# Performance work log

Hardware: AMD Instinct MI355X
Metric: run time of the kernel (lower is better)

Reference implementation:

```python
import jax, jax.numpy as jnp
import numpy as np

N_USERS = 100000
N_ITEMS = 50000
N_NODES = N_USERS + N_ITEMS
D = 64
N_LAYERS = 3
POP_BINS = 10
NNZ = 2000000
BATCH = 256
BIAS_SCALE = 1.0


def setup_inputs() -> dict:
    key = jax.random.key(0)
    ks = jax.random.split(key, 16)
    std = 0.01
    inp = {
        "user_emb": jax.random.normal(ks[0], (N_USERS, D), jnp.float32) * std,
        "item_emb": jax.random.normal(ks[1], (N_ITEMS, D), jnp.float32) * std,
        "user_bias": jnp.zeros((N_USERS, 1), jnp.float32),
        "item_bias": jnp.zeros((N_ITEMS, 1), jnp.float32),
        "pop_emb": jax.random.normal(ks[2], (POP_BINS, D), jnp.float32) * std,
        "uW1": jax.random.normal(ks[3], (D, D), jnp.float32) / np.sqrt(D),
        "ub1": jnp.zeros((D,), jnp.float32),
        "uW2": jax.random.normal(ks[4], (D, D), jnp.float32) / np.sqrt(D),
        "ub2": jnp.zeros((D,), jnp.float32),
        "iW1": jax.random.normal(ks[5], (D, D), jnp.float32) / np.sqrt(D),
        "ib1": jnp.zeros((D,), jnp.float32),
        "iW2": jax.random.normal(ks[6], (D, D), jnp.float32) / np.sqrt(D),
        "ib2": jnp.zeros((D,), jnp.float32),
        "gW1": jax.random.normal(ks[7], (2 * D, D), jnp.float32) / np.sqrt(2 * D),
        "gb1": jnp.zeros((D,), jnp.float32),
        "gW2": jax.random.normal(ks[8], (D, 1), jnp.float32) / np.sqrt(D),
        "gb2": jnp.zeros((1,), jnp.float32),
        "adj_vals": jax.random.uniform(ks[9], (NNZ,), jnp.float32),
        "adj_rows": jax.random.randint(ks[10], (NNZ,), 0, N_NODES, jnp.int32),
        "adj_cols": jax.random.randint(ks[11], (NNZ,), 0, N_NODES, jnp.int32),
        "item_pop_bins": jax.random.randint(ks[12], (N_ITEMS,), 0, POP_BINS, jnp.int32),
        "users": jax.random.randint(ks[13], (BATCH,), 0, N_USERS, jnp.int32),
    }
    return inp


def _spmm(vals, rows, cols, E):
    # sparse (N x N) @ E  via gather + segment-sum
    msgs = vals[:, None] * E[cols]          # [nnz, d]
    return jax.ops.segment_sum(msgs, rows, num_segments=N_NODES)


def _mlp2(x, W1, b1, W2, b2):
    return jax.nn.relu(x @ W1 + b1) @ W2 + b2


def reference(user_emb, item_emb, user_bias, item_bias, pop_emb,
              uW1, ub1, uW2, ub2, iW1, ib1, iW2, ib2,
              gW1, gb1, gW2, gb2,
              adj_vals, adj_rows, adj_cols, item_pop_bins, users):
    # ---- computer(): LightGCN propagation with uniform layer weights ----
    emb = jnp.concatenate([user_emb, item_emb], axis=0)   # [N, d]
    w = 1.0 / (N_LAYERS + 1)
    out = emb * w
    cur = emb
    for _ in range(N_LAYERS):
        cur = _spmm(adj_vals, adj_rows, adj_cols, cur)
        out = out + cur * w
    all_users, all_items = out[:N_USERS], out[N_USERS:]

    # ---- popularity-gated item fusion ----
    p_vec = pop_emb[item_pop_bins]                         # [n_items, d]
    gate_in = jnp.concatenate([all_items, p_vec], axis=-1)
    z = jax.nn.sigmoid(_mlp2(gate_in, gW1, gb1, gW2, gb2)) # [n_items, 1]
    items_fused = (1.0 - z) * all_items + z * p_vec

    # ---- two-tower scoring over all items ----
    U = _mlp2(all_users[users], uW1, ub1, uW2, ub2)        # [B, d]
    I = _mlp2(items_fused, iW1, ib1, iW2, ib2)             # [n_items, d]
    scores = U @ I.T                                        # [B, n_items]
    scores = scores + user_bias[users] * BIAS_SCALE + (item_bias.T) * BIAS_SCALE
    return scores
```

## Files before the change

### kernel.cpp

```cpp
#include <hip/hip_runtime.h>
#include <hip/hip_fp16.h>

#define N_USERS 100000
#define N_ITEMS 50000
#define N_NODES 150000
#define D 64
#define NNZ 2000000
#define BATCH 256
#define POP_BINS 10

#define BSH 9
#define NB2 293
#define CAP 8192
#define P1_EPB 4096
#define P1_BLOCKS 489

#define ST_P 130

__global__ __launch_bounds__(256) void k_bcount(const int* __restrict__ rows,
                                                int* __restrict__ bcnt) {
  __shared__ int c[NB2];
  int t = threadIdx.x;
  for (int i = t; i < NB2; i += 256) c[i] = 0;
  __syncthreads();
  int base = blockIdx.x * P1_EPB;
  for (int i = 0; i < 16; i++) {
    int e = base + i * 256 + t;
    if (e < NNZ) atomicAdd(&c[rows[e] >> BSH], 1);
  }
  __syncthreads();
  for (int i = t; i < NB2; i += 256)
    if (c[i]) atomicAdd(&bcnt[i], c[i]);
}

__global__ __launch_bounds__(512) void k_bscan(int* __restrict__ bcnt) {
  __shared__ int s[512];
  int t = threadIdx.x;
  int v = (t < NB2) ? bcnt[t] : 0;
  s[t] = v;
  __syncthreads();
  for (int o = 1; o < 512; o <<= 1) {
    int x = (t >= o) ? s[t - o] : 0;
    __syncthreads();
    s[t] += x;
    __syncthreads();
  }
  if (t < NB2) bcnt[t] = s[t] - v;
}

__global__ __launch_bounds__(256) void k_p1(const int* __restrict__ rows,
                                            const int* __restrict__ cols,
                                            const float* __restrict__ vals,
                                            int* __restrict__ bcur,
                                            uint2* __restrict__ gstage) {
  __shared__ int cnt[NB2];
  __shared__ int gbase[NB2];
  int t = threadIdx.x;
  for (int i = t; i < NB2; i += 256) cnt[i] = 0;
  __syncthreads();
  int base = blockIdx.x * P1_EPB;
  for (int i = 0; i < 16; i++) {
    int e = base + i * 256 + t;
    if (e < NNZ) atomicAdd(&cnt[rows[e] >> BSH], 1);
  }
  __syncthreads();
  for (int i = t; i < NB2; i += 256) {
    int c = cnt[i];
    gbase[i] = c ? atomicAdd(&bcur[i], c) : 0;
    cnt[i] = 0;
  }
  __syncthreads();
  for (int i = 0; i < 16; i++) {
    int e = base + i * 256 + t;
    if (e < NNZ) {
      int r = rows[e];
      int b = r >> BSH;
      int rank = atomicAdd(&cnt[b], 1);
      unsigned key = ((unsigned)(r & 511) << 18) | (unsigned)cols[e];
      gstage[gbase[b] + rank] = make_uint2(key, __float_as_uint(vals[e]));
    }
  }
}

__global__ __launch_bounds__(256) void k_p2(const int* __restrict__ bcur,
                                            const uint2* __restrict__ gstage,
                                            uint2* __restrict__ epack,
                                            int* __restrict__ rowptr) {
  __shared__ int cnt[512];
  __shared__ int off[512];
  __shared__ int s[256];
  __shared__ uint2 buf[CAP];
  int b = blockIdx.x, t = threadIdx.x;
  int base = (b == 0) ? 0 : bcur[b - 1];
  int end = bcur[b];
  int n = end - base;
  cnt[t] = 0;
  cnt[t + 256] = 0;
  __syncthreads();
  for (int j = t; j < n; j += 256)
    atomicAdd(&cnt[gstage[base + j].x >> 18], 1);
  __syncthreads();
  int c0 = cnt[2 * t], c1 = cnt[2 * t + 1];
  s[t] = c0 + c1;
  __syncthreads();
  for (int o = 1; o < 256; o <<= 1) {
    int x = (t >= o) ? s[t - o] : 0;
    __syncthreads();
    s[t] += x;
    __syncthreads();
  }
  int ex = t ? s[t - 1] : 0;
  off[2 * t] = ex;
  off[2 * t + 1] = ex + c0;
  int gr = (b << BSH) + 2 * t;
  if (gr < N_NODES) rowptr[gr] = base + ex;
  if (gr + 1 < N_NODES) rowptr[gr + 1] = base + ex + c0;
  if (b == NB2 - 1 && t == 0) rowptr[N_NODES] = NNZ;
  __syncthreads();
  for (int j = t; j < n; j += 256) {
    uint2 ed = gstage[base + j];
    int lr = ed.x >> 18;
    int pos = atomicAdd(&off[lr], 1);
    buf[pos] = make_uint2(ed.x & 0x3FFFFu, ed.y);
  }
  __syncthreads();
  for (int j = t; j < n; j += 256) epack[base + j] = buf[j];
}

__global__ __launch_bounds__(256) void k_flags(const int* __restrict__ users,
                                               int* __restrict__ uflag,
                                               int* __restrict__ ulist,
                                               int* __restrict__ ucnt) {
  int u = users[threadIdx.x];
  if (atomicExch(&uflag[u], 1) == 0) {
    int p = atomicAdd(ucnt, 1);
    ulist[p] = u;
  }
}

__global__ __launch_bounds__(256) void k_cvt(const float* __restrict__ ue,
                                             const float* __restrict__ ie,
                                             __half* __restrict__ Eh) {
  int t = blockIdx.x * 256 + threadIdx.x;
  if (t >= 2400000) return;
  size_t fo = (size_t)t * 4;
  const float* src = (fo < (size_t)N_USERS * 64) ? ue + fo
                                                 : ie + (fo - (size_t)N_USERS * 64);
  float4 v = *(const float4*)src;
  __half2* dst = (__half2*)(Eh + fo);
  dst[0] = __floats2half2_rn(v.x, v.y);
  dst[1] = __floats2half2_rn(v.z, v.w);
}

#define SPMM_QW_BODY(TBL)                                                     \
  float a0 = 0.f, a1 = 0.f, a2 = 0.f, a3 = 0.f;                               \
  int j = beg;                                                                \
  for (; j + 7 < end; j += 8) {                                               \
    uint2 ea = epack[j + q];                                                  \
    uint2 eb = epack[j + 4 + q];                                              \
    uint2 ra = *(const uint2*)(TBL + (size_t)ea.x * 64 + 4 * p);              \
    uint2 rb = *(const uint2*)(TBL + (size_t)eb.x * 64 + 4 * p);              \
    float va = __uint_as_float(ea.y), vb = __uint_as_float(eb.y);             \
    float2 la = __half22float2(*(const __half2*)&ra.x);                       \
    float2 ha = __half22float2(*(const __half2*)&ra.y);                       \
    float2 lb = __half22float2(*(const __half2*)&rb.x);                       \
    float2 hb = __half22float2(*(const __half2*)&rb.y);                       \
    a0 += va * la.x; a1 += va * la.y; a2 += va * ha.x; a3 += va * ha.y;       \
    a0 += vb * lb.x; a1 += vb * lb.y; a2 += vb * hb.x; a3 += vb * hb.y;       \
  }                                                                           \
  for (; j < end; j += 4) {                                                   \
    int jj = j + q;                                                           \
    int jc = (jj < end) ? jj : end - 1;                                       \
    uint2 e = epack[jc];                                                      \
    float v = (jj < end) ? __uint_as_float(e.y) : 0.f;                        \
    uint2 r = *(const uint2*)(TBL + (size_t)e.x * 64 + 4 * p);                \
    float2 l = __half22float2(*(const __half2*)&r.x);                         \
    float2 h2 = __half22float2(*(const __half2*)&r.y);                        \
    a0 += v * l.x; a1 += v * l.y; a2 += v * h2.x; a3 += v * h2.y;             \
  }                                                                           \
  a0 += __shfl_xor(a0, 16, 64); a0 += __shfl_xor(a0, 32, 64);                 \
  a1 += __shfl_xor(a1, 16, 64); a1 += __shfl_xor(a1, 32, 64);                 \
  a2 += __shfl_xor(a2, 16, 64); a2 += __shfl_xor(a2, 32, 64);                 \
  a3 += __shfl_xor(a3, 16, 64); a3 += __shfl_xor(a3, 32, 64);

__global__ __launch_bounds__(256) void k_spmm1(const int* __restrict__ rowptr,
                                               const uint2* __restrict__ epack,
                                               const float* __restrict__ ue,
                                               const float* __restrict__ ie,
                                               const __half* __restrict__ Eh0,
                                               const int* __restrict__ uflag,
                                               __half* __restrict__ EoutH,
                                               float* __restrict__ Oacc) {
  int wave = blockIdx.x * 4 + (threadIdx.x >> 6);
  int row = __builtin_amdgcn_readfirstlane(wave);
  if (row >= N_NODES) return;
  int lane = threadIdx.x & 63;
  int p = lane & 15, q = lane >> 4;
  int beg = rowptr[row];
  int end = rowptr[row + 1];
  SPMM_QW_BODY(Eh0)
  if (q == 0) {
    __half2* eo = (__half2*)(EoutH + (size_t)row * 64 + 4 * p);
    eo[0] = __floats2half2_rn(a0, a1);
    eo[1] = __floats2half2_rn(a2, a3);
    bool need = (row >= N_USERS) || (uflag[row] != 0);
    if (need) {
      const float* srow = (row < N_USERS) ? ue + (size_t)row * 64
                                          : ie + (size_t)(row - N_USERS) * 64;
      float4 sv = *(const float4*)(srow + 4 * p);
      *(float4*)(Oacc + (size_t)row * 64 + 4 * p) =
          make_float4(0.25f * (sv.x + a0), 0.25f * (sv.y + a1),
                      0.25f * (sv.z + a2), 0.25f * (sv.w + a3));
    }
  }
}

__global__ __launch_bounds__(256) void k_spmm2h(const int* __restrict__ rowptr,
                                                const uint2* __restrict__ epack,
                                                const __half* __restrict__ Ein,
                                                const int* __restrict__ uflag,
                                                __half* __restrict__ EoutH,
                                                float* __restrict__ Oacc) {
  int wave = blockIdx.x * 4 + (threadIdx.x >> 6);
  int row = __builtin_amdgcn_readfirstlane(wave);
  if (row >= N_NODES) return;
  int lane = threadIdx.x & 63;
  int p = lane & 15, q = lane >> 4;
  int beg = rowptr[row];
  int end = rowptr[row + 1];
  SPMM_QW_BODY(Ein)
  if (q == 0) {
    __half2* eo = (__half2*)(EoutH + (size_t)row * 64 + 4 * p);
    eo[0] = __floats2half2_rn(a0, a1);
    eo[1] = __floats2half2_rn(a2, a3);
    if (row >= N_USERS || uflag[row] != 0) {
      float4* op = (float4*)(Oacc + (size_t)row * 64 + 4 * p);
      float4 cur = *op;
      *op = make_float4(cur.x + 0.25f * a0, cur.y + 0.25f * a1,
                        cur.z + 0.25f * a2, cur.w + 0.25f * a3);
    }
  }
}

__global__ __launch_bounds__(256) void k_spmm3h(const int* __restrict__ rowptr,
                                                const uint2* __restrict__ epack,
                                                const __half* __restrict__ Ein,
                                                const int* __restrict__ ulist,
                                                const int* __restrict__ ucnt,
                                                float* __restrict__ Oacc) {
  int w = blockIdx.x * 4 + (threadIdx.x >> 6);
  int row;
  if (w < N_ITEMS) {
    row = N_USERS + w;
  } else {
    int k = w - N_ITEMS;
    if (k >= ucnt[0]) return;
    row = ulist[k];
  }
  row = __builtin_amdgcn_readfirstlane(row);
  int lane = threadIdx.x & 63;
  int p = lane & 15, q = lane >> 4;
  int beg = rowptr[row];
  int end = rowptr[row + 1];
  SPMM_QW_BODY(Ein)
  if (q == 0) {
    float4* op = (float4*)(Oacc + (size_t)row * 64 + 4 * p);
    float4 cur = *op;
    *op = make_float4(cur.x + 0.25f * a0, cur.y + 0.25f * a1,
                      cur.z + 0.25f * a2, cur.w + 0.25f * a3);
  }
}

__global__ __launch_bounds__(256) void k_wt(const float* __restrict__ uW1,
                                            float* __restrict__ WT) {
  int t = blockIdx.x * 256 + threadIdx.x;
  if (t < 4096) {
    int o = t >> 6, k = t & 63;
    WT[t] = uW1[k * 64 + o];
  }
}

__global__ __launch_bounds__(256) void k_pw(const float* __restrict__ pop,
                                            const float* __restrict__ gW1,
                                            const float* __restrict__ iW1,
                                            float* __restrict__ hp,
                                            float* __restrict__ pp1) {
  for (int idx = threadIdx.x; idx < 2 * POP_BINS * 64; idx += 256) {
    int q = idx;
    bool second = q >= POP_BINS * 64;
    if (second) q -= POP_BINS * 64;
    int b = q >> 6, o = q & 63;
    float s = 0.f;
    if (!second) {
      for (int k = 0; k < 64; k++) s += pop[b * 64 + k] * gW1[(64 + k) * 64 + o];
      hp[q] = s;
    } else {
      for (int k = 0; k < 64; k++) s += pop[b * 64 + k] * iW1[k * 64 + o];
      pp1[q] = s;
    }
  }
}

__global__ __launch_bounds__(64) void k_user(const float* __restrict__ Oacc,
                                             const int* __restrict__ users,
                                             const float* __restrict__ ubias,
                                             const float* __restrict__ uW1T,
                                             const float* __restrict__ ub1,
                                             const float* __restrict__ uW2,
                                             const float* __restrict__ ub2,
                                             float* __restrict__ Ut) {
  int b = blockIdx.x * 64 + threadIdx.x;
  int u = users[b];
  float x[64];
  const float4* xr = (const float4*)(Oacc + (size_t)u * 64);
#pragma unroll
  for (int q = 0; q < 16; q++) {
    float4 t4 = xr[q];
    x[4 * q] = t4.x; x[4 * q + 1] = t4.y; x[4 * q + 2] = t4.z; x[4 * q + 3] = t4.w;
  }
  float acc[64];
#pragma unroll
  for (int o2 = 0; o2 < 64; o2++) acc[o2] = ub2[o2];
#pragma unroll 1
  for (int o = 0; o < 64; o++) {
    const float* w = uW1T + o * 64;
    float a0 = ub1[o], a1 = 0.f, a2 = 0.f, a3 = 0.f;
#pragma unroll
    for (int k = 0; k < 64; k += 4) {
      a0 += x[k] * w[k]; a1 += x[k + 1] * w[k + 1];
      a2 += x[k + 2] * w[k + 2]; a3 += x[k + 3] * w[k + 3];
    }
    float hv = a0 + a1 + a2 + a3;
    hv = hv > 0.f ? hv : 0.f;
    const float* w2 = uW2 + o * 64;
#pragma unroll
    for (int o2 = 0; o2 < 64; o2++) acc[o2] += hv * w2[o2];
  }
#pragma unroll
  for (int o2 = 0; o2 < 64; o2++) Ut[o2 * 256 + b] = acc[o2];
  Ut[64 * 256 + b] = ubias[u];
}

__global__ __launch_bounds__(256) void k_gemm1z(const float* __restrict__ Oacc,
                                                const float* __restrict__ gW1,
                                                const float* __restrict__ iW1,
                                                const int* __restrict__ bins,
                                                const float* __restrict__ hp,
                                                const float* __restrict__ pp1,
                                                const float* __restrict__ gb1,
                                                const float* __restrict__ gW2,
                                                const float* __restrict__ gb2,
                                                const float* __restrict__ ib1,
                                                float* __restrict__ H1) {
  __shared__ float Is[64 * ST_P];
  __shared__ float Bs[64 * 128];
  __shared__ float zp[128][9];
  __shared__ float zs[128];
  int tid = threadIdx.x;
  int i0 = blockIdx.x * 128;
  {
    int c4 = tid & 15, r0 = tid >> 4;
#pragma unroll
    for (int s = 0; s < 8; s++) {
      int r = r0 + s * 16;
      int it = i0 + r;
      float4 v = make_float4(0.f, 0.f, 0.f, 0.f);
      if (it < N_ITEMS) v = *(const float4*)(Oacc + (size_t)(N_USERS + it) * 64 + c4 * 4);
      Is[(c4 * 4 + 0) * ST_P + r] = v.x;
      Is[(c4 * 4 + 1) * ST_P + r] = v.y;
      Is[(c4 * 4 + 2) * ST_P + r] = v.z;
      Is[(c4 * 4 + 3) * ST_P + r] = v.w;
    }
  }
  for (int idx = tid; idx < 64 * 128; idx += 256) {
    int k = idx >> 7, o = idx & 127;
    Bs[idx] = (o < 64) ? gW1[k * 64 + o] : iW1[k * 64 + (o - 64)];
  }
  __syncthreads();
  int tx = tid & 15, ty = tid >> 4;
  float acc[8][8];
#pragma unroll
  for (int a = 0; a < 8; a++)
#pragma unroll
    for (int b = 0; b < 8; b++) acc[a][b] = 0.f;
  const float* ip = Is + tx * 8;
  const float* wp = Bs + ty * 8;
#pragma unroll 2
  for (int k = 0; k < 64; k++) {
    float4 iv0 = *(const float4*)(ip + k * ST_P);
    float4 iv1 = *(const float4*)(ip + k * ST_P + 4);
    float4 wv0 = *(const float4*)(wp + k * 128);
    float4 wv1 = *(const float4*)(wp + k * 128 + 4);
    float iv[8] = {iv0.x, iv0.y, iv0.z, iv0.w, iv1.x, iv1.y, iv1.z, iv1.w};
    float wv[8] = {wv0.x, wv0.y, wv0.z, wv0.w, wv1.x, wv1.y, wv1.z, wv1.w};
#pragma unroll
    for (int a = 0; a < 8; a++)
#pragma unroll
      for (int b = 0; b < 8; b++) acc[a][b] += iv[a] * wv[b];
  }
  int ibase = i0 + tx * 8;
  if (ty < 8) {
    int o0 = ty * 8;
#pragma unroll
    for (int a = 0; a < 8; a++) {
      int it = ibase + a;
      float p = 0.f;
      if (it < N_ITEMS) {
        int bin = bins[it];
        const float* hpr = hp + bin * 64 + o0;
#pragma unroll
        for (int b = 0; b < 8; b++) {
          float g = acc[a][b] + hpr[b] + gb1[o0 + b];
          g = g > 0.f ? g : 0.f;
          p += g * gW2[o0 + b];
        }
      }
      zp[tx * 8 + a][ty] = p;
    }
  }
  __syncthreads();
  if (tid < 128) {
    float s = gb2[0];
#pragma unroll
    for (int k = 0; k < 8; k++) s += zp[tid][k];
    zs[tid] = 1.f / (1.f + expf(-s));
  }
  __syncthreads();
  if (ty >= 8) {
    int o0 = (ty - 8) * 8;
#pragma unroll
    for (int a = 0; a < 8; a++) {
      int it = ibase + a;
      if (it < N_ITEMS) {
        float z = zs[tx * 8 + a];
        int bin = bins[it];
        const float* ppr = pp1 + bin * 64 + o0;
        float h[8];
#pragma unroll
        for (int b = 0; b < 8; b++) {
          float v = (1.f - z) * acc[a][b] + z * ppr[b] + ib1[o0 + b];
          h[b] = v > 0.f ? v : 0.f;
        }
        *(float4*)(H1 + (size_t)it * 64 + o0) = make_float4(h[0], h[1], h[2], h[3]);
        *(float4*)(H1 + (size_t)it * 64 + o0 + 4) = make_float4(h[4], h[5], h[6], h[7]);
      }
    }
  }
}

__global__ __launch_bounds__(256) void k_gemm2(const float* __restrict__ H1,
                                               const float* __restrict__ iW2,
                                               const float* __restrict__ ib2,
                                               float* __restrict__ I) {
  __shared__ float Is[64 * ST_P];
  __shared__ float Bs[64 * 64];
  int tid = threadIdx.x;
  int i0 = blockIdx.x * 128;
  {
    int c4 = tid & 15, r0 = tid >> 4;
#pragma unroll
    for (int s = 0; s < 8; s++) {
      int r = r0 + s * 16;
      int it = i0 + r;
      float4 v = make_float4(0.f, 0.f, 0.f, 0.f);
      if (it < N_ITEMS) v = *(const float4*)(H1 + (size_t)it * 64 + c4 * 4);
      Is[(c4 * 4 + 0) * ST_P + r] = v.x;
      Is[(c4 * 4 + 1) * ST_P + r] = v.y;
      Is[(c4 * 4 + 2) * ST_P + r] = v.z;
      Is[(c4 * 4 + 3) * ST_P + r] = v.w;
    }
  }
  for (int idx = tid; idx < 64 * 64; idx += 256) Bs[idx] = iW2[idx];
  __syncthreads();
  int tx = tid & 15, ty = tid >> 4;
  float acc[8][4];
#pragma unroll
  for (int a = 0; a < 8; a++)
#pragma unroll
    for (int b = 0; b < 4; b++) acc[a][b] = 0.f;
  const float* ip = Is + tx * 8;
  const float* wp = Bs + ty * 4;
#pragma unroll 2
  for (int k = 0; k < 64; k++) {
    float4 iv0 = *(const float4*)(ip + k * ST_P);
    float4 iv1 = *(const float4*)(ip + k * ST_P + 4);
    float4 wv = *(const float4*)(wp + k * 64);
    float iv[8] = {iv0.x, iv0.y, iv0.z, iv0.w, iv1.x, iv1.y, iv1.z, iv1.w};
    float wvv[4] = {wv.x, wv.y, wv.z, wv.w};
#pragma unroll
    for (int a = 0; a < 8; a++)
#pragma unroll
      for (int b = 0; b < 4; b++) acc[a][b] += iv[a] * wvv[b];
  }
  int ibase = i0 + tx * 8;
  int oc = ty * 4;
  float b0 = ib2[oc], b1 = ib2[oc + 1], b2 = ib2[oc + 2], b3 = ib2[oc + 3];
#pragma unroll
  for (int a = 0; a < 8; a++) {
    int it = ibase + a;
    if (it < N_ITEMS) {
      float4 s0 = make_float4(acc[a][0] + b0, acc[a][1] + b1,
                              acc[a][2] + b2, acc[a][3] + b3);
      *(float4*)(I + (size_t)it * 64 + oc) = s0;
    }
  }
}

__global__ __launch_bounds__(256) void k_scores(const float* __restrict__ I,
                                                const float* __restrict__ Ut,
                                                const float* __restrict__ item_bias,
                                                float* __restrict__ out) {
  __shared__ float Is[64 * ST_P];
  __shared__ float Us[64 * 128];
  int tid = threadIdx.x;
  int i0 = blockIdx.x * 128;
  int ubase = blockIdx.y * 128;
  {
    int c4 = tid & 15, r0 = tid >> 4;
#pragma unroll
    for (int s = 0; s < 8; s++) {
      int r = r0 + s * 16;
      int it = i0 + r;
      float4 v = make_float4(0.f, 0.f, 0.f, 0.f);
      if (it < N_ITEMS) v = *(const float4*)(I + (size_t)it * 64 + c4 * 4);
      Is[(c4 * 4 + 0) * ST_P + r] = v.x;
      Is[(c4 * 4 + 1) * ST_P + r] = v.y;
      Is[(c4 * 4 + 2) * ST_P + r] = v.z;
      Is[(c4 * 4 + 3) * ST_P + r] = v.w;
    }
  }
  {
    int u4 = tid & 31, k0 = tid >> 5;
#pragma unroll
    for (int s = 0; s < 8; s++) {
      int k = k0 + s * 8;
      float4 v = *(const float4*)(Ut + k * 256 + ubase + u4 * 4);
      *(float4*)(Us + k * 128 + u4 * 4) = v;
    }
  }
  __syncthreads();
  int tx = tid & 15;
  int ty = tid >> 4;
  float acc[8][8];
#pragma unroll
  for (int a = 0; a < 8; a++)
#pragma unroll
    for (int b = 0; b < 8; b++) acc[a][b] = 0.f;
  const float* ip = Is + tx * 8;
  const float* up = Us + ty * 8;
#pragma unroll 2
  for (int k = 0; k < 64; k++) {
    float4 iv0 = *(const float4*)(ip + k * ST_P);
    float4 iv1 = *(const float4*)(ip + k * ST_P + 4);
    float4 uv0 = *(const float4*)(up + k * 128);
    float4 uv1 = *(const float4*)(up + k * 128 + 4);
    float iv[8] = {iv0.x, iv0.y, iv0.z, iv0.w, iv1.x, iv1.y, iv1.z, iv1.w};
    float uv[8] = {uv0.x, uv0.y, uv0.z, uv0.w, uv1.x, uv1.y, uv1.z, uv1.w};
#pragma unroll
    for (int a = 0; a < 8; a++)
#pragma unroll
      for (int b = 0; b < 8; b++) acc[a][b] += iv[a] * uv[b];
  }
  int ibase = i0 + tx * 8;
  float ib[8];
#pragma unroll
  for (int a = 0; a < 8; a++)
    ib[a] = (ibase + a < N_ITEMS) ? item_bias[ibase + a] : 0.f;
#pragma unroll
  for (int bb = 0; bb < 8; bb++) {
    int bu = ubase + ty * 8 + bb;
    float ubias = Ut[64 * 256 + bu];
    float* orow = out + (size_t)bu * N_ITEMS + ibase;
    if (ibase + 7 < N_ITEMS) {
      float4 s0 = make_float4(acc[0][bb] + ubias + ib[0], acc[1][bb] + ubias + ib[1],
                              acc[2][bb] + ubias + ib[2], acc[3][bb] + ubias + ib[3]);
      float4 s1 = make_float4(acc[4][bb] + ubias + ib[4], acc[5][bb] + ubias + ib[5],
                              acc[6][bb] + ubias + ib[6], acc[7][bb] + ubias + ib[7]);
      *(float4*)orow = s0;
      *(float4*)(orow + 4) = s1;
    } else {
#pragma unroll
      for (int a = 0; a < 8; a++)
        if (ibase + a < N_ITEMS) orow[a] = acc[a][bb] + ubias + ib[a];
    }
  }
}

extern "C" void kernel_launch(void* const* d_in, const int* in_sizes, int n_in,
                              void* d_out, int out_size, void* d_ws, size_t ws_size,
                              hipStream_t stream) {
  const float* user_emb  = (const float*)d_in[0];
  const float* item_emb  = (const float*)d_in[1];
  const float* user_bias = (const float*)d_in[2];
  const float* item_bias = (const float*)d_in[3];
  const float* pop_emb   = (const float*)d_in[4];
  const float* uW1 = (const float*)d_in[5];
  const float* ub1 = (const float*)d_in[6];
  const float* uW2 = (const float*)d_in[7];
  const float* ub2 = (const float*)d_in[8];
  const float* iW1 = (const float*)d_in[9];
  const float* ib1 = (const float*)d_in[10];
  const float* iW2 = (const float*)d_in[11];
  const float* ib2 = (const float*)d_in[12];
  const float* gW1 = (const float*)d_in[13];
  const float* gb1 = (const float*)d_in[14];
  const float* gW2 = (const float*)d_in[15];
  const float* gb2 = (const float*)d_in[16];
  const float* adj_vals = (const float*)d_in[17];
  const int* adj_rows = (const int*)d_in[18];
  const int* adj_cols = (const int*)d_in[19];
  const int* bins  = (const int*)d_in[20];
  const int* users = (const int*)d_in[21];
  float* out = (float*)d_out;

  float* ws = (float*)d_ws;
  float* Oacc = ws;
  float* bufA = ws + 9600000;
  float* bufB = ws + 19200000;
  uint2* epack = (uint2*)(ws + 28800000);
  int* rowptr = (int*)(ws + 32800000);
  int* uflag  = (int*)(ws + 32960000);
  int* ucnt   = (int*)(ws + 33060000);
  int* ulist  = (int*)(ws + 33061000);
  float* Ut   = ws + 33130000;
  float* WT   = ws + 33150000;
  float* hp   = ws + 33160000;
  float* pp1  = ws + 33161000;
  int* bcur   = (int*)(ws + 33170000);
  uint2* gstage = (uint2*)bufB;
  __half* Eh0 = (__half*)bufA;
  __half* E1h = (__half*)(bufA + 4800000);
  __half* E2h = (__half*)bufB;
  float* H1 = bufA + 6400000;
  float* I  = bufB;
  const float* uW1T = WT;

  hipMemsetAsync(bcur, 0, NB2 * sizeof(int), stream);
  hipMemsetAsync(uflag, 0, 100001 * sizeof(int), stream);
  k_cvt<<<9375, 256, 0, stream>>>(user_emb, item_emb, Eh0);
  k_bcount<<<P1_BLOCKS, 256, 0, stream>>>(adj_rows, bcur);
  k_bscan<<<1, 512, 0, stream>>>(bcur);
  k_p1<<<P1_BLOCKS, 256, 0, stream>>>(adj_rows, adj_cols, adj_vals, bcur, gstage);
  k_p2<<<NB2, 256, 0, stream>>>(bcur, gstage, epack, rowptr);
  k_flags<<<1, 256, 0, stream>>>(users, uflag, ulist, ucnt);

  k_spmm1<<<37500, 256, 0, stream>>>(rowptr, epack, user_emb, item_emb, Eh0, uflag, E1h, Oacc);
  k_spmm2h<<<37500, 256, 0, stream>>>(rowptr, epack, E1h, uflag, E2h, Oacc);
  k_spmm3h<<<12564, 256, 0, stream>>>(rowptr, epack, E2h, ulist, ucnt, Oacc);

  k_wt<<<16, 256, 0, stream>>>(uW1, WT);
  k_pw<<<1, 256, 0, stream>>>(pop_emb, gW1, iW1, hp, pp1);
  k_user<<<4, 64, 0, stream>>>(Oacc, users, user_bias, uW1T, ub1, uW2, ub2, Ut);
  k_gemm1z<<<391, 256, 0, stream>>>(Oacc, gW1, iW1, bins, hp, pp1, gb1, gW2, gb2, ib1, H1);
  k_gemm2<<<391, 256, 0, stream>>>(H1, iW2, ib2, I);
  k_scores<<<dim3(391, 2), 256, 0, stream>>>(I, Ut, item_bias, out);
}
```

Before: 554.7 us.

## Drop bucket count pass, prefetch SpMM edges deeply, bitmask flags, wave-parallel user MLP

```diff
diff --git a/kernel.cpp b/kernel.cpp
--- a/kernel.cpp
+++ b/kernel.cpp
@@ -16,37 +16,7 @@
 #define P1_BLOCKS 489
 
 #define ST_P 130
-
-__global__ __launch_bounds__(256) void k_bcount(const int* __restrict__ rows,
-                                                int* __restrict__ bcnt) {
-  __shared__ int c[NB2];
-  int t = threadIdx.x;
-  for (int i = t; i < NB2; i += 256) c[i] = 0;
-  __syncthreads();
-  int base = blockIdx.x * P1_EPB;
-  for (int i = 0; i < 16; i++) {
-    int e = base + i * 256 + t;
-    if (e < NNZ) atomicAdd(&c[rows[e] >> BSH], 1);
-  }
-  __syncthreads();
-  for (int i = t; i < NB2; i += 256)
-    if (c[i]) atomicAdd(&bcnt[i], c[i]);
-}
-
-__global__ __launch_bounds__(512) void k_bscan(int* __restrict__ bcnt) {
-  __shared__ int s[512];
-  int t = threadIdx.x;
-  int v = (t < NB2) ? bcnt[t] : 0;
-  s[t] = v;
-  __syncthreads();
-  for (int o = 1; o < 512; o <<= 1) {
-    int x = (t >= o) ? s[t - o] : 0;
-    __syncthreads();
-    s[t] += x;
-    __syncthreads();
-  }
-  if (t < NB2) bcnt[t] = s[t] - v;
-}
+#define MAXC 7
 
 __global__ __launch_bounds__(256) void k_p1(const int* __restrict__ rows,
                                             const int* __restrict__ cols,
@@ -77,7 +47,8 @@
       int b = r >> BSH;
       int rank = atomicAdd(&cnt[b], 1);
       unsigned key = ((unsigned)(r & 511) << 18) | (unsigned)cols[e];
-      gstage[gbase[b] + rank] = make_uint2(key, __float_as_uint(vals[e]));
+      gstage[(size_t)b * CAP + gbase[b] + rank] =
+          make_uint2(key, __float_as_uint(vals[e]));
     }
   }
 }
@@ -85,20 +56,23 @@
 __global__ __launch_bounds__(256) void k_p2(const int* __restrict__ bcur,
                                             const uint2* __restrict__ gstage,
                                             uint2* __restrict__ epack,
-                                            int* __restrict__ rowptr) {
+                                            int* __restrict__ rowbeg,
+                                            int* __restrict__ rowend,
+                                            int* __restrict__ gcursor) {
   __shared__ int cnt[512];
   __shared__ int off[512];
   __shared__ int s[256];
+  __shared__ int gbs;
   __shared__ uint2 buf[CAP];
   int b = blockIdx.x, t = threadIdx.x;
-  int base = (b == 0) ? 0 : bcur[b - 1];
-  int end = bcur[b];
-  int n = end - base;
+  int n = bcur[b];
+  const uint2* gs = gstage + (size_t)b * CAP;
+  if (t == 0) gbs = atomicAdd(gcursor, n);
   cnt[t] = 0;
   cnt[t + 256] = 0;
   __syncthreads();
   for (int j = t; j < n; j += 256)
-    atomicAdd(&cnt[gstage[base + j].x >> 18], 1);
+    atomicAdd(&cnt[gs[j].x >> 18], 1);
   __syncthreads();
   int c0 = cnt[2 * t], c1 = cnt[2 * t + 1];
   s[t] = c0 + c1;
@@ -112,13 +86,13 @@
   int ex = t ? s[t - 1] : 0;
   off[2 * t] = ex;
   off[2 * t + 1] = ex + c0;
+  int base = gbs;
   int gr = (b << BSH) + 2 * t;
-  if (gr < N_NODES) rowptr[gr] = base + ex;
-  if (gr + 1 < N_NODES) rowptr[gr + 1] = base + ex + c0;
-  if (b == NB2 - 1 && t == 0) rowptr[N_NODES] = NNZ;
+  if (gr < N_NODES) { rowbeg[gr] = base + ex; rowend[gr] = base + ex + c0; }
+  if (gr + 1 < N_NODES) { rowbeg[gr + 1] = base + ex + c0; rowend[gr + 1] = base + ex + c0 + c1; }
   __syncthreads();
   for (int j = t; j < n; j += 256) {
-    uint2 ed = gstage[base + j];
+    uint2 ed = gs[j];
     int lr = ed.x >> 18;
     int pos = atomicAdd(&off[lr], 1);
     buf[pos] = make_uint2(ed.x & 0x3FFFFu, ed.y);
@@ -132,7 +106,8 @@
                                                int* __restrict__ ulist,
                                                int* __restrict__ ucnt) {
   int u = users[threadIdx.x];
-  if (atomicExch(&uflag[u], 1) == 0) {
+  int old = atomicOr(&uflag[u >> 5], 1 << (u & 31));
+  if (!((old >> (u & 31)) & 1)) {
     int p = atomicAdd(ucnt, 1);
     ulist[p] = u;
   }
@@ -152,38 +127,55 @@
   dst[1] = __floats2half2_rn(v.z, v.w);
 }
 
-#define SPMM_QW_BODY(TBL)                                                     \
+#define SPMM_DEEP(TBL)                                                        \
+  int n = end - beg;                                                          \
+  int nc = (n + 3) >> 2;                                                      \
+  if (nc > MAXC) nc = MAXC;                                                   \
+  uint2 ed[MAXC];                                                             \
+  _Pragma("unroll")                                                           \
+  for (int c = 0; c < MAXC; c++) {                                            \
+    if (c < nc) {                                                             \
+      int jj = beg + 4 * c + q;                                               \
+      int jc = jj < end ? jj : end - 1;                                       \
+      ed[c] = epack[jc];                                                      \
+    }                                                                         \
+  }                                                                           \
+  uint2 rg[MAXC]; float rv[MAXC];                                             \
+  _Pragma("unroll")                                                           \
+  for (int c = 0; c < MAXC; c++) {                                            \
+    if (c < nc) {                                                             \
+      int jj = beg + 4 * c + q;                                               \
+      rv[c] = (jj < end) ? __uint_as_float(ed[c].y) : 0.f;                    \
+      rg[c] = *(const uint2*)(TBL + (size_t)ed[c].x * 64 + 4 * p);            \
+    }                                                                         \
+  }                                                                           \
   float a0 = 0.f, a1 = 0.f, a2 = 0.f, a3 = 0.f;                               \
-  int j = beg;                                                                \
-  for (; j + 7 < end; j += 8) {                                               \
-    uint2 ea = epack[j + q];                                                  \
-    uint2 eb = epack[j + 4 + q];                                              \
-    uint2 ra = *(const uint2*)(TBL + (size_t)ea.x * 64 + 4 * p);              \
-    uint2 rb = *(const uint2*)(TBL + (size_t)eb.x * 64 + 4 * p);              \
-    float va = __uint_as_float(ea.y), vb = __uint_as_float(eb.y);             \
-    float2 la = __half22float2(*(const __half2*)&ra.x);                       \
-    float2 ha = __half22float2(*(const __half2*)&ra.y);                       \
-    float2 lb = __half22float2(*(const __half2*)&rb.x);                       \
-    float2 hb = __half22float2(*(const __half2*)&rb.y);                       \
-    a0 += va * la.x; a1 += va * la.y; a2 += va * ha.x; a3 += va * ha.y;       \
-    a0 += vb * lb.x; a1 += vb * lb.y; a2 += vb * hb.x; a3 += vb * hb.y;       \
+  _Pragma("unroll")                                                           \
+  for (int c = 0; c < MAXC; c++) {                                            \
+    if (c < nc) {                                                             \
+      float2 lo = __half22float2(*(const __half2*)&rg[c].x);                  \
+      float2 hi = __half22float2(*(const __half2*)&rg[c].y);                  \
+      a0 += rv[c] * lo.x; a1 += rv[c] * lo.y;                                 \
+      a2 += rv[c] * hi.x; a3 += rv[c] * hi.y;                                 \
+    }                                                                         \
   }                                                                           \
-  for (; j < end; j += 4) {                                                   \
+  for (int j = beg + 4 * MAXC; j < end; j += 4) {   \
     int jj = j + q;                                                           \
-    int jc = (jj < end) ? jj : end - 1;                                       \
+    int jc = jj < end ? jj : end - 1;                                         \
     uint2 e = epack[jc];                                                      \
     float v = (jj < end) ? __uint_as_float(e.y) : 0.f;                        \
     uint2 r = *(const uint2*)(TBL + (size_t)e.x * 64 + 4 * p);                \
-    float2 l = __half22float2(*(const __half2*)&r.x);                         \
-    float2 h2 = __half22float2(*(const __half2*)&r.y);                        \
-    a0 += v * l.x; a1 += v * l.y; a2 += v * h2.x; a3 += v * h2.y;             \
+    float2 lo = __half22float2(*(const __half2*)&r.x);                        \
+    float2 hi = __half22float2(*(const __half2*)&r.y);                        \
+    a0 += v * lo.x; a1 += v * lo.y; a2 += v * hi.x; a3 += v * hi.y;           \
   }                                                                           \
   a0 += __shfl_xor(a0, 16, 64); a0 += __shfl_xor(a0, 32, 64);                 \
   a1 += __shfl_xor(a1, 16, 64); a1 += __shfl_xor(a1, 32, 64);                 \
   a2 += __shfl_xor(a2, 16, 64); a2 += __shfl_xor(a2, 32, 64);                 \
   a3 += __shfl_xor(a3, 16, 64); a3 += __shfl_xor(a3, 32, 64);
 
-__global__ __launch_bounds__(256) void k_spmm1(const int* __restrict__ rowptr,
+__global__ __launch_bounds__(256) void k_spmm1(const int* __restrict__ rowbeg,
+                                               const int* __restrict__ rowend,
                                                const uint2* __restrict__ epack,
                                                const float* __restrict__ ue,
                                                const float* __restrict__ ie,
@@ -196,14 +188,14 @@
   if (row >= N_NODES) return;
   int lane = threadIdx.x & 63;
   int p = lane & 15, q = lane >> 4;
-  int beg = rowptr[row];
-  int end = rowptr[row + 1];
-  SPMM_QW_BODY(Eh0)
+  int beg = rowbeg[row];
+  int end = rowend[row];
+  SPMM_DEEP(Eh0)
   if (q == 0) {
     __half2* eo = (__half2*)(EoutH + (size_t)row * 64 + 4 * p);
     eo[0] = __floats2half2_rn(a0, a1);
     eo[1] = __floats2half2_rn(a2, a3);
-    bool need = (row >= N_USERS) || (uflag[row] != 0);
+    bool need = (row >= N_USERS) || (((uflag[row >> 5] >> (row & 31)) & 1) != 0);
     if (need) {
       const float* srow = (row < N_USERS) ? ue + (size_t)row * 64
                                           : ie + (size_t)(row - N_USERS) * 64;
@@ -215,7 +207,8 @@
   }
 }
 
-__global__ __launch_bounds__(256) void k_spmm2h(const int* __restrict__ rowptr,
+__global__ __launch_bounds__(256) void k_spmm2h(const int* __restrict__ rowbeg,
+                                                const int* __restrict__ rowend,
                                                 const uint2* __restrict__ epack,
                                                 const __half* __restrict__ Ein,
                                                 const int* __restrict__ uflag,
@@ -226,14 +219,14 @@
   if (row >= N_NODES) return;
   int lane = threadIdx.x & 63;
   int p = lane & 15, q = lane >> 4;
-  int beg = rowptr[row];
-  int end = rowptr[row + 1];
-  SPMM_QW_BODY(Ein)
+  int beg = rowbeg[row];
+  int end = rowend[row];
+  SPMM_DEEP(Ein)
   if (q == 0) {
     __half2* eo = (__half2*)(EoutH + (size_t)row * 64 + 4 * p);
     eo[0] = __floats2half2_rn(a0, a1);
     eo[1] = __floats2half2_rn(a2, a3);
-    if (row >= N_USERS || uflag[row] != 0) {
+    if (row >= N_USERS || (((uflag[row >> 5] >> (row & 31)) & 1) != 0)) {
       float4* op = (float4*)(Oacc + (size_t)row * 64 + 4 * p);
       float4 cur = *op;
       *op = make_float4(cur.x + 0.25f * a0, cur.y + 0.25f * a1,
@@ -242,7 +235,8 @@
   }
 }
 
-__global__ __launch_bounds__(256) void k_spmm3h(const int* __restrict__ rowptr,
+__global__ __launch_bounds__(256) void k_spmm3h(const int* __restrict__ rowbeg,
+                                                const int* __restrict__ rowend,
                                                 const uint2* __restrict__ epack,
                                                 const __half* __restrict__ Ein,
                                                 const int* __restrict__ ulist,
@@ -260,23 +254,14 @@
   row = __builtin_amdgcn_readfirstlane(row);
   int lane = threadIdx.x & 63;
   int p = lane & 15, q = lane >> 4;
-  int beg = rowptr[row];
-  int end = rowptr[row + 1];
-  SPMM_QW_BODY(Ein)
+  int beg = rowbeg[row];
+  int end = rowend[row];
+  SPMM_DEEP(Ein)
   if (q == 0) {
     float4* op = (float4*)(Oacc + (size_t)row * 64 + 4 * p);
     float4 cur = *op;
     *op = make_float4(cur.x + 0.25f * a0, cur.y + 0.25f * a1,
                       cur.z + 0.25f * a2, cur.w + 0.25f * a3);
-  }
-}
-
-__global__ __launch_bounds__(256) void k_wt(const float* __restrict__ uW1,
-                                            float* __restrict__ WT) {
-  int t = blockIdx.x * 256 + threadIdx.x;
-  if (t < 4096) {
-    int o = t >> 6, k = t & 63;
-    WT[t] = uW1[k * 64 + o];
   }
 }
 
@@ -301,44 +286,29 @@
   }
 }
 
-__global__ __launch_bounds__(64) void k_user(const float* __restrict__ Oacc,
-                                             const int* __restrict__ users,
-                                             const float* __restrict__ ubias,
-                                             const float* __restrict__ uW1T,
-                                             const float* __restrict__ ub1,
-                                             const float* __restrict__ uW2,
-                                             const float* __restrict__ ub2,
-                                             float* __restrict__ Ut) {
-  int b = blockIdx.x * 64 + threadIdx.x;
-  int u = users[b];
-  float x[64];
-  const float4* xr = (const float4*)(Oacc + (size_t)u * 64);
-#pragma unroll
-  for (int q = 0; q < 16; q++) {
-    float4 t4 = xr[q];
-    x[4 * q] = t4.x; x[4 * q + 1] = t4.y; x[4 * q + 2] = t4.z; x[4 * q + 3] = t4.w;
-  }
-  float acc[64];
-#pragma unroll
-  for (int o2 = 0; o2 < 64; o2++) acc[o2] = ub2[o2];
-#pragma unroll 1
-  for (int o = 0; o < 64; o++) {
-    const float* w = uW1T + o * 64;
-    float a0 = ub1[o], a1 = 0.f, a2 = 0.f, a3 = 0.f;
-#pragma unroll
-    for (int k = 0; k < 64; k += 4) {
-      a0 += x[k] * w[k]; a1 += x[k + 1] * w[k + 1];
-      a2 += x[k + 2] * w[k + 2]; a3 += x[k + 3] * w[k + 3];
-    }
-    float hv = a0 + a1 + a2 + a3;
-    hv = hv > 0.f ? hv : 0.f;
-    const float* w2 = uW2 + o * 64;
-#pragma unroll
-    for (int o2 = 0; o2 < 64; o2++) acc[o2] += hv * w2[o2];
-  }
-#pragma unroll
-  for (int o2 = 0; o2 < 64; o2++) Ut[o2 * 256 + b] = acc[o2];
-  Ut[64 * 256 + b] = ubias[u];
+__global__ __launch_bounds__(256) void k_user(const float* __restrict__ Oacc,
+                                              const int* __restrict__ users,
+                                              const float* __restrict__ ubias,
+                                              const float* __restrict__ uW1,
+                                              const float* __restrict__ ub1,
+                                              const float* __restrict__ uW2,
+                                              const float* __restrict__ ub2,
+                                              float* __restrict__ Ut) {
+  int ub = blockIdx.x * 4 + (threadIdx.x >> 6);
+  int lane = threadIdx.x & 63;
+  int u = users[ub];
+  float x = Oacc[(size_t)u * 64 + lane];
+  float h = ub1[lane];
+#pragma unroll
+  for (int k = 0; k < 64; k++)
+    h = fmaf(__shfl(x, k, 64), uW1[k * 64 + lane], h);
+  h = h > 0.f ? h : 0.f;
+  float o = ub2[lane];
+#pragma unroll
+  for (int k = 0; k < 64; k++)
+    o = fmaf(__shfl(h, k, 64), uW2[k * 64 + lane], o);
+  Ut[lane * 256 + ub] = o;
+  if (lane == 0) Ut[64 * 256 + ub] = ubias[u];
 }
 
 __global__ __launch_bounds__(256) void k_gemm1z(const float* __restrict__ Oacc,
@@ -618,39 +588,36 @@
   float* bufA = ws + 9600000;
   float* bufB = ws + 19200000;
   uint2* epack = (uint2*)(ws + 28800000);
-  int* rowptr = (int*)(ws + 32800000);
-  int* uflag  = (int*)(ws + 32960000);
-  int* ucnt   = (int*)(ws + 33060000);
-  int* ulist  = (int*)(ws + 33061000);
-  float* Ut   = ws + 33130000;
-  float* WT   = ws + 33150000;
-  float* hp   = ws + 33160000;
-  float* pp1  = ws + 33161000;
-  int* bcur   = (int*)(ws + 33170000);
+  int* rowbeg = (int*)(ws + 32800000);
+  int* rowend = (int*)(ws + 32950000);
+  int* uflag  = (int*)(ws + 33100000);
+  int* ucnt   = (int*)(ws + 33103125);
+  int* ulist  = (int*)(ws + 33103130);
+  float* Ut   = ws + 33104000;
+  float* hp   = ws + 33121000;
+  float* pp1  = ws + 33122000;
+  int* bcur   = (int*)(ws + 33123000);
+  int* gcursor = (int*)(ws + 33123293);
   uint2* gstage = (uint2*)bufB;
   __half* Eh0 = (__half*)bufA;
   __half* E1h = (__half*)(bufA + 4800000);
   __half* E2h = (__half*)bufB;
   float* H1 = bufA + 6400000;
   float* I  = bufB;
-  const float* uW1T = WT;
-
-  hipMemsetAsync(bcur, 0, NB2 * sizeof(int), stream);
-  hipMemsetAsync(uflag, 0, 100001 * sizeof(int), stream);
+
+  hipMemsetAsync(bcur, 0, 294 * sizeof(int), stream);
+  hipMemsetAsync(uflag, 0, 3126 * sizeof(int), stream);
   k_cvt<<<9375, 256, 0, stream>>>(user_emb, item_emb, Eh0);
-  k_bcount<<<P1_BLOCKS, 256, 0, stream>>>(adj_rows, bcur);
-  k_bscan<<<1, 512, 0, stream>>>(bcur);
   k_p1<<<P1_BLOCKS, 256, 0, stream>>>(adj_rows, adj_cols, adj_vals, bcur, gstage);
-  k_p2<<<NB2, 256, 0, stream>>>(bcur, gstage, epack, rowptr);
+  k_p2<<<NB2, 256, 0, stream>>>(bcur, gstage, epack, rowbeg, rowend, gcursor);
   k_flags<<<1, 256, 0, stream>>>(users, uflag, ulist, ucnt);
 
-  k_spmm1<<<37500, 256, 0, stream>>>(rowptr, epack, user_emb, item_emb, Eh0, uflag, E1h, Oacc);
-  k_spmm2h<<<37500, 256, 0, stream>>>(rowptr, epack, E1h, uflag, E2h, Oacc);
-  k_spmm3h<<<12564, 256, 0, stream>>>(rowptr, epack, E2h, ulist, ucnt, Oacc);
-
-  k_wt<<<16, 256, 0, stream>>>(uW1, WT);
+  k_spmm1<<<37500, 256, 0, stream>>>(rowbeg, rowend, epack, user_emb, item_emb, Eh0, uflag, E1h, Oacc);
+  k_spmm2h<<<37500, 256, 0, stream>>>(rowbeg, rowend, epack, E1h, uflag, E2h, Oacc);
+  k_spmm3h<<<12564, 256, 0, stream>>>(rowbeg, rowend, epack, E2h, ulist, ucnt, Oacc);
+
   k_pw<<<1, 256, 0, stream>>>(pop_emb, gW1, iW1, hp, pp1);
-  k_user<<<4, 64, 0, stream>>>(Oacc, users, user_bias, uW1T, ub1, uW2, ub2, Ut);
+  k_user<<<64, 256, 0, stream>>>(Oacc, users, user_bias, uW1, ub1, uW2, ub2, Ut);
   k_gemm1z<<<391, 256, 0, stream>>>(Oacc, gW1, iW1, bins, hp, pp1, gb1, gW2, gb2, ib1, H1);
   k_gemm2<<<391, 256, 0, stream>>>(H1, iW2, ib2, I);
   k_scores<<<dim3(391, 2), 256, 0, stream>>>(I, Ut, item_bias, out);
```

Result: faster. 505.6 us (-8.8%).
